# Optimization experiments

Hardware: AMD Instinct MI355X
Metric: run time of the kernel (lower is better)

The kernel has to match this reference:

```python
import jax, jax.numpy as jnp
import numpy as np

FEATS = 1024
HEAD = 16
MLP_HIDDEN = 4096
HEAD_DIM = FEATS // HEAD
SQRT_D = float(FEATS) ** 0.5  # module scales by sqrt(feats), not sqrt(head_dim)
LN_EPS = 1e-5


def layer_norm(x, g, b):
    mu = jnp.mean(x, axis=-1, keepdims=True)
    var = jnp.mean(jnp.square(x - mu), axis=-1, keepdims=True)
    return (x - mu) * jax.lax.rsqrt(var + LN_EPS) * g + b


def setup_inputs() -> dict:
    key = jax.random.key(0)
    ks = jax.random.split(key, 12)
    s = 1.0 / np.sqrt(FEATS)
    s2 = 1.0 / np.sqrt(MLP_HIDDEN)
    return {
        "x": jax.random.normal(ks[0], (2, 2048, FEATS), dtype=jnp.float32),
        "ln1_g": jnp.ones((FEATS,), jnp.float32),
        "ln1_b": jnp.zeros((FEATS,), jnp.float32),
        "wq": jax.random.normal(ks[1], (FEATS, FEATS), jnp.float32) * s,
        "bq": jnp.zeros((FEATS,), jnp.float32),
        "wk": jax.random.normal(ks[2], (FEATS, FEATS), jnp.float32) * s,
        "bk": jnp.zeros((FEATS,), jnp.float32),
        "wv": jax.random.normal(ks[3], (FEATS, FEATS), jnp.float32) * s,
        "bv": jnp.zeros((FEATS,), jnp.float32),
        "wo": jax.random.normal(ks[4], (FEATS, FEATS), jnp.float32) * s,
        "bo": jnp.zeros((FEATS,), jnp.float32),
        "ln2_g": jnp.ones((FEATS,), jnp.float32),
        "ln2_b": jnp.zeros((FEATS,), jnp.float32),
        "w1": jax.random.normal(ks[5], (MLP_HIDDEN, FEATS), jnp.float32) * s,
        "b1": jnp.zeros((MLP_HIDDEN,), jnp.float32),
        "w2": jax.random.normal(ks[6], (FEATS, MLP_HIDDEN), jnp.float32) * s2,
        "b2": jnp.zeros((FEATS,), jnp.float32),
    }


def reference(x, ln1_g, ln1_b, wq, bq, wk, bk, wv, bv, wo, bo,
              ln2_g, ln2_b, w1, b1, w2, b2):
    b, n, f = x.shape
    h = layer_norm(x, ln1_g, ln1_b)
    # qkv projections (torch Linear: y = x @ W.T + b)
    q = (h @ wq.T + bq).reshape(b, n, HEAD, HEAD_DIM).transpose(0, 2, 1, 3)
    k = (h @ wk.T + bk).reshape(b, n, HEAD, HEAD_DIM).transpose(0, 2, 1, 3)
    v = (h @ wv.T + bv).reshape(b, n, HEAD, HEAD_DIM).transpose(0, 2, 1, 3)
    score = jax.nn.softmax(jnp.einsum('bhif,bhjf->bhij', q, k) / SQRT_D, axis=-1)
    attn = jnp.einsum('bhij,bhjf->bihf', score, v).reshape(b, n, f)
    o = attn @ wo.T + bo
    out1 = o + x
    h2 = layer_norm(out1, ln2_g, ln2_b)
    mlp = jax.nn.relu(jax.nn.relu(h2 @ w1.T + b1) @ w2.T + b2)
    return mlp + out1
```

## Files before the change

kernel.cpp:

```cpp
#include <hip/hip_runtime.h>
#include <hip/hip_bf16.h>

#define FEATS 1024
#define NH 16
#define HD 64
#define SEQ 2048
#define BATCH 2
#define MTOT (BATCH*SEQ)
#define MLPH 4096

typedef __attribute__((ext_vector_type(8))) short bf16x8;
typedef __attribute__((ext_vector_type(4))) float f32x4;

static_assert(sizeof(bf16x8) == 16, "bf16x8 must be 16B");

__device__ __forceinline__ unsigned short f2bf(float f) {
    unsigned int u = __float_as_uint(f);
    unsigned int lsb = (u >> 16) & 1u;
    u += 0x7fffu + lsb;
    return (unsigned short)(u >> 16);
}

#define ASYNC16(GP, LP) __builtin_amdgcn_global_load_lds( \
    (const __attribute__((address_space(1))) void*)(GP),  \
    (__attribute__((address_space(3))) void*)(LP), 16, 0, 0)

__global__ __launch_bounds__(256) void cvt_kernel(const float* __restrict__ src,
                                                  unsigned short* __restrict__ dst, int n) {
    int i = (blockIdx.x * 256 + threadIdx.x) * 4;
    if (i + 3 < n) {
        float4 v = *(const float4*)(src + i);
        ushort4 o;
        o.x = f2bf(v.x); o.y = f2bf(v.y); o.z = f2bf(v.z); o.w = f2bf(v.w);
        *(ushort4*)(dst + i) = o;
    }
}

__global__ __launch_bounds__(256) void concat3_kernel(const float* __restrict__ a,
                                                      const float* __restrict__ b,
                                                      const float* __restrict__ c,
                                                      float* __restrict__ o) {
    int i = blockIdx.x * 256 + threadIdx.x;
    float v = (i < 1024) ? a[i] : ((i < 2048) ? b[i - 1024] : c[i - 2048]);
    o[i] = v;
}

__global__ __launch_bounds__(256) void ln_kernel(const float* __restrict__ x,
                                                 const float* __restrict__ g,
                                                 const float* __restrict__ bta,
                                                 unsigned short* __restrict__ h) {
    __shared__ float red[8];
    const int row = blockIdx.x;
    const int t = threadIdx.x;
    const float* xr = x + (size_t)row * FEATS;
    float4 v = ((const float4*)xr)[t];
    float s  = v.x + v.y + v.z + v.w;
    float ss = v.x * v.x + v.y * v.y + v.z * v.z + v.w * v.w;
#pragma unroll
    for (int off = 1; off < 64; off <<= 1) {
        s  += __shfl_xor(s, off);
        ss += __shfl_xor(ss, off);
    }
    const int w = t >> 6;
    if ((t & 63) == 0) { red[w] = s; red[4 + w] = ss; }
    __syncthreads();
    s  = red[0] + red[1] + red[2] + red[3];
    ss = red[4] + red[5] + red[6] + red[7];
    const float mu  = s * (1.f / FEATS);
    const float var = ss * (1.f / FEATS) - mu * mu;
    const float rs  = rsqrtf(var + 1e-5f);
    float4 gv = ((const float4*)g)[t];
    float4 bv = ((const float4*)bta)[t];
    ushort4 ov;
    ov.x = f2bf((v.x - mu) * rs * gv.x + bv.x);
    ov.y = f2bf((v.y - mu) * rs * gv.y + bv.y);
    ov.z = f2bf((v.z - mu) * rs * gv.z + bv.z);
    ov.w = f2bf((v.w - mu) * rs * gv.w + bv.w);
    ((ushort4*)h)[(size_t)row * (FEATS / 4) + t] = ov;
}

template <bool RELU, bool ADD, bool OUTBF16>
__global__ __launch_bounds__(256, 2)
void gemm_kernel(const unsigned short* __restrict__ A,
                 const unsigned short* __restrict__ W,
                 const float* __restrict__ bias,
                 const float* __restrict__ addend,
                 void* __restrict__ outp,
                 int M, int N, int K, int gx) {
    __shared__ unsigned short lds[3][2][128 * 32];

    const int t = threadIdx.x;
    const int w = t >> 6, lane = t & 63;
    const int wr = w >> 1, wc = w & 1;
    const int li = lane & 15, lj = lane >> 4;

    const int nwg = gridDim.x;
    const int cpx = nwg >> 3;
    const int wg = blockIdx.x;
    const int swz = (wg & 7) * cpx + (wg >> 3);
    const int mb = (swz / gx) * 128, nb = (swz % gx) * 128;

    const int srow = lane >> 2, sc = (lane & 3) * 8;
    const unsigned short* gA = A + (size_t)(mb + w * 16 + srow) * K + sc;
    const unsigned short* gB = W + (size_t)(nb + w * 16 + srow) * K + sc;
    const size_t half = (size_t)64 * K;
    const int lbase = w * 512 + lane * 8;

    const int nt = K >> 5;

#define STAGE(BUF, K0)                                             \
    do {                                                           \
        unsigned short* la_ = &lds[BUF][0][lbase];                 \
        unsigned short* lb_ = &lds[BUF][1][lbase];                 \
        ASYNC16(gA + (K0), la_);                                   \
        ASYNC16(gA + half + (K0), la_ + 2048);                     \
        ASYNC16(gB + (K0), lb_);                                   \
        ASYNC16(gB + half + (K0), lb_ + 2048);                     \
    } while (0)

    STAGE(0, 0);
    STAGE(1, 32);
    asm volatile("s_waitcnt vmcnt(4)" ::: "memory");
    __builtin_amdgcn_s_barrier();

    f32x4 acc[4][4] = {};

    for (int i = 0; i < nt; ++i) {
        const int cur = i % 3;
        const unsigned short* Al = &lds[cur][0][0];
        const unsigned short* Bl = &lds[cur][1][0];

        bf16x8 af[4], bfr[4];
#pragma unroll
        for (int m = 0; m < 4; m++)
            af[m] = *(const bf16x8*)(Al + (wr * 64 + m * 16 + li) * 32 + lj * 8);
#pragma unroll
        for (int n = 0; n < 4; n++)
            bfr[n] = *(const bf16x8*)(Bl + (wc * 64 + n * 16 + li) * 32 + lj * 8);

        const int pf = i + 2 < nt;
        if (pf) STAGE((i + 2) % 3, (i + 2) * 32);

#pragma unroll
        for (int m = 0; m < 4; m++)
#pragma unroll
            for (int n = 0; n < 4; n++)
                acc[m][n] = __builtin_amdgcn_mfma_f32_16x16x32_bf16(af[m], bfr[n], acc[m][n], 0, 0, 0);

        if (i + 1 < nt) {
            if (pf) asm volatile("s_waitcnt vmcnt(4)" ::: "memory");
            else    asm volatile("s_waitcnt vmcnt(0)" ::: "memory");
            __builtin_amdgcn_s_barrier();
        }
    }
#undef STAGE

#pragma unroll
    for (int m = 0; m < 4; m++) {
#pragma unroll
        for (int n = 0; n < 4; n++) {
            const int col = nb + wc * 64 + n * 16 + li;
            const float bv = bias[col];
#pragma unroll
            for (int r = 0; r < 4; r++) {
                const int row = mb + wr * 64 + m * 16 + lj * 4 + r;
                float v = acc[m][n][r] + bv;
                if (RELU) v = fmaxf(v, 0.f);
                if (ADD)  v += addend[(size_t)row * N + col];
                if (OUTBF16)
                    ((unsigned short*)outp)[(size_t)row * N + col] = f2bf(v);
                else
                    ((float*)outp)[(size_t)row * N + col] = v;
            }
        }
    }
}

__global__ __launch_bounds__(256) void vtrans_kernel(const unsigned short* __restrict__ qkv,
                                                     unsigned short* __restrict__ vt) {
    constexpr int LDV = 68;
    __shared__ unsigned short Vl[64 * LDV];
    const int bh = blockIdx.x, st = blockIdx.y;
    const int b = bh >> 4, h = bh & 15;
    const int t = threadIdx.x;
    const unsigned short* src = qkv + (size_t)(b * SEQ + st * 64) * (3 * FEATS) + 2 * FEATS + h * HD;
#pragma unroll
    for (int i = 0; i < 2; i++) {
        int idx = t + i * 256;
        int r = idx >> 3, c = (idx & 7) * 8;
        *(bf16x8*)(Vl + r * LDV + c) = *(const bf16x8*)(src + (size_t)r * (3 * FEATS) + c);
    }
    __syncthreads();
    unsigned short* dst = vt + (size_t)bh * HD * SEQ + st * 64;
#pragma unroll
    for (int i = 0; i < 2; i++) {
        int idx = t + i * 256;
        int d = idx >> 3, s8 = (idx & 7) * 8;
        bf16x8 v;
#pragma unroll
        for (int j = 0; j < 8; j++) v[j] = Vl[(s8 + j) * LDV + d];
        *(bf16x8*)(dst + (size_t)d * SEQ + s8) = v;
    }
}

__global__ __launch_bounds__(512, 2)
void attn_kernel(const unsigned short* __restrict__ qkv,
                 const unsigned short* __restrict__ vt,
                 unsigned short* __restrict__ out) {
    constexpr int LK = 72;
    constexpr int LP = 68;
    __shared__ unsigned short Kl[64 * LK];
    __shared__ unsigned short Vtl[64 * LK];
    __shared__ unsigned short Pl[8][16 * LP];

    const int bh = blockIdx.x;
    const int b = bh >> 4, h = bh & 15;
    const int q0 = blockIdx.y * 128;
    const int t = threadIdx.x, w = t >> 6, lane = t & 63;
    const int li = lane & 15, lj = lane >> 4;

    const size_t rstr = 3 * FEATS;
    const unsigned short* qkvb = qkv + (size_t)(b * SEQ) * rstr;
    const unsigned short* ksrc = qkvb + FEATS + h * HD;
    const unsigned short* vsrc = vt + (size_t)bh * HD * SEQ;

    bf16x8 aq[2];
#pragma unroll
    for (int kk = 0; kk < 2; kk++)
        aq[kk] = *(const bf16x8*)(qkvb + (size_t)(q0 + w * 16 + li) * rstr + h * HD + kk * 32 + lj * 8);

    f32x4 o[4] = {};
    float lsum[4] = {0.f, 0.f, 0.f, 0.f};
    const float c2 = 1.4426950408889634f / 32.0f;

    const int sr = t >> 3, scol = (t & 7) * 8;

    for (int kv0 = 0; kv0 < SEQ; kv0 += 64) {
        __syncthreads();
        *(bf16x8*)(Kl + sr * LK + scol) =
            *(const bf16x8*)(ksrc + (size_t)(kv0 + sr) * rstr + scol);
        *(bf16x8*)(Vtl + sr * LK + scol) =
            *(const bf16x8*)(vsrc + (size_t)sr * SEQ + kv0 + scol);
        __syncthreads();

        f32x4 s[4];
#pragma unroll
        for (int n = 0; n < 4; n++) {
            bf16x8 b0 = *(const bf16x8*)(Kl + (n * 16 + li) * LK + lj * 8);
            bf16x8 b1 = *(const bf16x8*)(Kl + (n * 16 + li) * LK + 32 + lj * 8);
            f32x4 acc = {};
            acc = __builtin_amdgcn_mfma_f32_16x16x32_bf16(aq[0], b0, acc, 0, 0, 0);
            acc = __builtin_amdgcn_mfma_f32_16x16x32_bf16(aq[1], b1, acc, 0, 0, 0);
            s[n] = acc;
        }

#pragma unroll
        for (int n = 0; n < 4; n++)
#pragma unroll
            for (int r = 0; r < 4; r++) {
                float p = exp2f(s[n][r] * c2);
                lsum[r] += p;
                Pl[w][(lj * 4 + r) * LP + n * 16 + li] = f2bf(p);
            }

#pragma unroll
        for (int kk = 0; kk < 2; kk++) {
            bf16x8 ap = *(const bf16x8*)(Pl[w] + li * LP + kk * 32 + lj * 8);
#pragma unroll
            for (int n = 0; n < 4; n++) {
                bf16x8 bv = *(const bf16x8*)(Vtl + (n * 16 + li) * LK + kk * 32 + lj * 8);
                o[n] = __builtin_amdgcn_mfma_f32_16x16x32_bf16(ap, bv, o[n], 0, 0, 0);
            }
        }
    }

    float inv[4];
#pragma unroll
    for (int r = 0; r < 4; r++) {
        float s = lsum[r];
        s += __shfl_xor(s, 1);
        s += __shfl_xor(s, 2);
        s += __shfl_xor(s, 4);
        s += __shfl_xor(s, 8);
        inv[r] = 1.f / s;
    }
    unsigned short* ob = out + (size_t)(b * SEQ + q0 + w * 16) * FEATS + h * HD;
#pragma unroll
    for (int n = 0; n < 4; n++)
#pragma unroll
        for (int r = 0; r < 4; r++)
            ob[(size_t)(lj * 4 + r) * FEATS + n * 16 + li] = f2bf(o[n][r] * inv[r]);
}

extern "C" void kernel_launch(void* const* d_in, const int* in_sizes, int n_in,
                              void* d_out, int out_size, void* d_ws, size_t ws_size,
                              hipStream_t stream) {
    const float* x     = (const float*)d_in[0];
    const float* ln1_g = (const float*)d_in[1];
    const float* ln1_b = (const float*)d_in[2];
    const float* wq    = (const float*)d_in[3];
    const float* bq    = (const float*)d_in[4];
    const float* wk    = (const float*)d_in[5];
    const float* bk    = (const float*)d_in[6];
    const float* wv    = (const float*)d_in[7];
    const float* bvv   = (const float*)d_in[8];
    const float* wo    = (const float*)d_in[9];
    const float* bo    = (const float*)d_in[10];
    const float* ln2_g = (const float*)d_in[11];
    const float* ln2_b = (const float*)d_in[12];
    const float* w1    = (const float*)d_in[13];
    const float* b1    = (const float*)d_in[14];
    const float* w2    = (const float*)d_in[15];
    const float* b2    = (const float*)d_in[16];

    unsigned short* wqkv_b = (unsigned short*)d_ws;
    unsigned short* wo_b   = wqkv_b + 3072 * 1024;
    unsigned short* w1_b   = wo_b + 1024 * 1024;
    unsigned short* w2_b   = w1_b + 4096 * 1024;
    float*          bqkv   = (float*)(w2_b + 1024 * 4096);
    unsigned short* region = (unsigned short*)(bqkv + 3072);
    unsigned short* qkvb   = region;
    unsigned short* hb     = region + (size_t)4096 * 3072;
    unsigned short* vtb    = hb;
    unsigned short* a1     = region;
    unsigned short* attn_o = region + (size_t)4096 * 4096;
    unsigned short* h2     = attn_o;
    float*          out1   = (float*)(attn_o + (size_t)4096 * 1024);
    float*          outf   = (float*)d_out;

    dim3 blk(256);

    cvt_kernel<<<1024, blk, 0, stream>>>(wq, wqkv_b, 1024 * 1024);
    cvt_kernel<<<1024, blk, 0, stream>>>(wk, wqkv_b + 1024 * 1024, 1024 * 1024);
    cvt_kernel<<<1024, blk, 0, stream>>>(wv, wqkv_b + 2 * 1024 * 1024, 1024 * 1024);
    cvt_kernel<<<1024, blk, 0, stream>>>(wo, wo_b, 1024 * 1024);
    cvt_kernel<<<4096, blk, 0, stream>>>(w1, w1_b, 4096 * 1024);
    cvt_kernel<<<4096, blk, 0, stream>>>(w2, w2_b, 4096 * 1024);
    concat3_kernel<<<12, blk, 0, stream>>>(bq, bk, bvv, bqkv);

    ln_kernel<<<MTOT, blk, 0, stream>>>(x, ln1_g, ln1_b, hb);

    gemm_kernel<false, false, true><<<768, blk, 0, stream>>>(
        hb, wqkv_b, bqkv, nullptr, qkvb, MTOT, 3072, FEATS, 24);

    vtrans_kernel<<<dim3(BATCH * NH, SEQ / 64), blk, 0, stream>>>(qkvb, vtb);

    attn_kernel<<<dim3(BATCH * NH, SEQ / 128), dim3(512), 0, stream>>>(qkvb, vtb, attn_o);

    gemm_kernel<false, true, false><<<256, blk, 0, stream>>>(
        attn_o, wo_b, bo, x, out1, MTOT, FEATS, FEATS, 8);

    ln_kernel<<<MTOT, blk, 0, stream>>>(out1, ln2_g, ln2_b, h2);

    gemm_kernel<true, false, true><<<1024, blk, 0, stream>>>(
        h2, w1_b, b1, nullptr, a1, MTOT, MLPH, FEATS, 32);

    gemm_kernel<true, true, false><<<256, blk, 0, stream>>>(
        a1, w2_b, b2, out1, outf, MTOT, FEATS, MLPH, 8);
}
```

Baseline: 262.9 us.

## Triple-buffer attention K/V tiles with async LDS loads and transposed P reads

Reworks the attention inner loop to stage K and V^T tiles into a three-deep LDS ring using async global-to-LDS loads, prefetching two tiles ahead. This replaces the synchronous load-then-barrier pattern, aiming to hide global latency. It also adds XOR-swizzled LDS layouts in place of padding, packed bf16 conversion of P, ds_read_b64_tr_b16 transposed reads for the P operand, and priority hints around the MFMA sections. Launch bounds are raised to 4 blocks per CU, which constrains registers and relies on the LDS footprint fitting, with added complexity in the waitcnt accounting.

Result: no change. 266.3 us (+1.3%).

```diff
diff --git a/kernel.cpp b/kernel.cpp
--- a/kernel.cpp
+++ b/kernel.cpp
@@ -10,6 +10,7 @@
 #define MLPH 4096
 
 typedef __attribute__((ext_vector_type(8))) short bf16x8;
+typedef __attribute__((ext_vector_type(4))) short bf16x4;
 typedef __attribute__((ext_vector_type(4))) float f32x4;
 
 static_assert(sizeof(bf16x8) == 16, "bf16x8 must be 16B");
@@ -203,26 +204,35 @@
     }
 }
 
-__global__ __launch_bounds__(512, 2)
+__global__ __launch_bounds__(512, 4)
 void attn_kernel(const unsigned short* __restrict__ qkv,
                  const unsigned short* __restrict__ vt,
                  unsigned short* __restrict__ out) {
-    constexpr int LK = 72;
-    constexpr int LP = 68;
-    __shared__ unsigned short Kl[64 * LK];
-    __shared__ unsigned short Vtl[64 * LK];
-    __shared__ unsigned short Pl[8][16 * LP];
+    __shared__ unsigned short Kl[3][64 * 64];
+    __shared__ unsigned short Vtl[3][64 * 64];
+    __shared__ unsigned short Pt[8][64 * 16];
 
     const int bh = blockIdx.x;
     const int b = bh >> 4, h = bh & 15;
     const int q0 = blockIdx.y * 128;
     const int t = threadIdx.x, w = t >> 6, lane = t & 63;
     const int li = lane & 15, lj = lane >> 4;
+    const int e7 = li & 7;
 
     const size_t rstr = 3 * FEATS;
     const unsigned short* qkvb = qkv + (size_t)(b * SEQ) * rstr;
-    const unsigned short* ksrc = qkvb + FEATS + h * HD;
-    const unsigned short* vsrc = vt + (size_t)bh * HD * SEQ;
+
+    const int sr = t >> 3;
+    const int sslot = (t & 7) ^ (sr & 7);
+    const unsigned short* kBase = qkvb + FEATS + h * HD + (size_t)sr * rstr + sslot * 8;
+    const unsigned short* vBase = vt + (size_t)bh * HD * SEQ + (size_t)sr * SEQ + sslot * 8;
+    const int ldst = t * 8;
+
+#define STAGEA(BUF, KV0)                                    \
+    do {                                                    \
+        ASYNC16(kBase + (size_t)(KV0) * rstr, &Kl[BUF][ldst]); \
+        ASYNC16(vBase + (KV0), &Vtl[BUF][ldst]);            \
+    } while (0)
 
     bf16x8 aq[2];
 #pragma unroll
@@ -233,56 +243,105 @@
     float lsum[4] = {0.f, 0.f, 0.f, 0.f};
     const float c2 = 1.4426950408889634f / 32.0f;
 
-    const int sr = t >> 3, scol = (t & 7) * 8;
-
-    for (int kv0 = 0; kv0 < SEQ; kv0 += 64) {
-        __syncthreads();
-        *(bf16x8*)(Kl + sr * LK + scol) =
-            *(const bf16x8*)(ksrc + (size_t)(kv0 + sr) * rstr + scol);
-        *(bf16x8*)(Vtl + sr * LK + scol) =
-            *(const bf16x8*)(vsrc + (size_t)sr * SEQ + kv0 + scol);
-        __syncthreads();
+    unsigned short* Ptw = &Pt[w][0];
+    const unsigned ptoff =
+        (unsigned)(size_t)(__attribute__((address_space(3))) void*)Ptw;
+    const unsigned paddr = ptoff + (unsigned)(li * 2 + lj * 128);
+
+    const int nt = SEQ / 64;
+    STAGEA(0, 0);
+    STAGEA(1, 64);
+    asm volatile("s_waitcnt vmcnt(2)" ::: "memory");
+    __builtin_amdgcn_s_barrier();
+
+    for (int i = 0; i < nt; ++i) {
+        const unsigned short* Kc = Kl[i % 3];
+        const unsigned short* Vc = Vtl[i % 3];
+
+        const int pf = i + 2 < nt;
+        if (pf) STAGEA((i + 2) % 3, (i + 2) * 64);
 
         f32x4 s[4];
+        __builtin_amdgcn_s_setprio(1);
 #pragma unroll
         for (int n = 0; n < 4; n++) {
-            bf16x8 b0 = *(const bf16x8*)(Kl + (n * 16 + li) * LK + lj * 8);
-            bf16x8 b1 = *(const bf16x8*)(Kl + (n * 16 + li) * LK + 32 + lj * 8);
+            const int row = n * 16 + li;
+            bf16x8 b0 = *(const bf16x8*)(Kc + row * 64 + ((lj ^ e7) * 8));
+            bf16x8 b1 = *(const bf16x8*)(Kc + row * 64 + (((lj + 4) ^ e7) * 8));
             f32x4 acc = {};
             acc = __builtin_amdgcn_mfma_f32_16x16x32_bf16(aq[0], b0, acc, 0, 0, 0);
             acc = __builtin_amdgcn_mfma_f32_16x16x32_bf16(aq[1], b1, acc, 0, 0, 0);
             s[n] = acc;
         }
-
-#pragma unroll
-        for (int n = 0; n < 4; n++)
-#pragma unroll
-            for (int r = 0; r < 4; r++) {
-                float p = exp2f(s[n][r] * c2);
-                lsum[r] += p;
-                Pl[w][(lj * 4 + r) * LP + n * 16 + li] = f2bf(p);
+        __builtin_amdgcn_s_setprio(0);
+
+#pragma unroll
+        for (int n = 0; n < 4; n++) {
+            float p0 = exp2f(s[n][0] * c2);
+            float p1 = exp2f(s[n][1] * c2);
+            float p2 = exp2f(s[n][2] * c2);
+            float p3 = exp2f(s[n][3] * c2);
+            lsum[0] += p0; lsum[1] += p1; lsum[2] += p2; lsum[3] += p3;
+            unsigned w0, w1;
+            asm("v_cvt_pk_bf16_f32 %0, %1, %2" : "=v"(w0) : "v"(p0), "v"(p1));
+            asm("v_cvt_pk_bf16_f32 %0, %1, %2" : "=v"(w1) : "v"(p2), "v"(p3));
+            uint2 pk; pk.x = w0; pk.y = w1;
+            *(uint2*)(Ptw + (n * 16 + li) * 16 + lj * 4) = pk;
+        }
+
+        asm volatile("s_waitcnt lgkmcnt(0)" ::: "memory");
+        __builtin_amdgcn_sched_barrier(0);
+        bf16x4 pa0, pa1, pa2, pa3;
+        asm volatile("ds_read_b64_tr_b16 %0, %4 offset:0\n\t"
+                     "ds_read_b64_tr_b16 %1, %4 offset:512\n\t"
+                     "ds_read_b64_tr_b16 %2, %4 offset:1024\n\t"
+                     "ds_read_b64_tr_b16 %3, %4 offset:1536"
+                     : "=&v"(pa0), "=&v"(pa1), "=&v"(pa2), "=&v"(pa3)
+                     : "v"(paddr));
+        bf16x8 A0 = __builtin_shufflevector(pa0, pa1, 0, 1, 2, 3, 4, 5, 6, 7);
+        bf16x8 A1 = __builtin_shufflevector(pa2, pa3, 0, 1, 2, 3, 4, 5, 6, 7);
+
+        bf16x8 bv[4][2];
+#pragma unroll
+        for (int n = 0; n < 4; n++) {
+            const int row = n * 16 + li;
+#pragma unroll
+            for (int kk = 0; kk < 2; kk++) {
+                bf16x4 vlo = *(const bf16x4*)(Vc + row * 64 +
+                    (((kk * 4 + (lj >> 1)) ^ e7) * 8) + (lj & 1) * 4);
+                bf16x4 vhi = *(const bf16x4*)(Vc + row * 64 +
+                    (((kk * 4 + 2 + (lj >> 1)) ^ e7) * 8) + (lj & 1) * 4);
+                bv[n][kk] = __builtin_shufflevector(vlo, vhi, 0, 1, 2, 3, 4, 5, 6, 7);
             }
-
-#pragma unroll
-        for (int kk = 0; kk < 2; kk++) {
-            bf16x8 ap = *(const bf16x8*)(Pl[w] + li * LP + kk * 32 + lj * 8);
-#pragma unroll
-            for (int n = 0; n < 4; n++) {
-                bf16x8 bv = *(const bf16x8*)(Vtl + (n * 16 + li) * LK + kk * 32 + lj * 8);
-                o[n] = __builtin_amdgcn_mfma_f32_16x16x32_bf16(ap, bv, o[n], 0, 0, 0);
-            }
-        }
-    }
+        }
+        asm volatile("s_waitcnt lgkmcnt(0)" ::: "memory");
+        __builtin_amdgcn_sched_barrier(0);
+
+        __builtin_amdgcn_s_setprio(1);
+#pragma unroll
+        for (int n = 0; n < 4; n++) {
+            o[n] = __builtin_amdgcn_mfma_f32_16x16x32_bf16(A0, bv[n][0], o[n], 0, 0, 0);
+            o[n] = __builtin_amdgcn_mfma_f32_16x16x32_bf16(A1, bv[n][1], o[n], 0, 0, 0);
+        }
+        __builtin_amdgcn_s_setprio(0);
+
+        if (i + 1 < nt) {
+            if (pf) asm volatile("s_waitcnt vmcnt(2)" ::: "memory");
+            else    asm volatile("s_waitcnt vmcnt(0)" ::: "memory");
+            __builtin_amdgcn_s_barrier();
+        }
+    }
+#undef STAGEA
 
     float inv[4];
 #pragma unroll
     for (int r = 0; r < 4; r++) {
-        float s = lsum[r];
-        s += __shfl_xor(s, 1);
-        s += __shfl_xor(s, 2);
-        s += __shfl_xor(s, 4);
-        s += __shfl_xor(s, 8);
-        inv[r] = 1.f / s;
+        float sred = lsum[r];
+        sred += __shfl_xor(sred, 1);
+        sred += __shfl_xor(sred, 2);
+        sred += __shfl_xor(sred, 4);
+        sred += __shfl_xor(sred, 8);
+        inv[r] = 1.f / sred;
     }
     unsigned short* ob = out + (size_t)(b * SEQ + q0 + w * 16) * FEATS + h * HD;
 #pragma unroll
```

## Double-buffer K/V tiles in attention with register prefetch and raise occupancy bounds

Applied to the files above, without the earlier changes.

The attention kernel now keeps two LDS buffers for K and V^T and loads the next tile into registers while the current tile is computed, then stores it to the other buffer. This cuts the per-iteration pair of barriers to one and hides global load latency behind the MFMA work. It also raises launch_bounds minimum occupancy for the GEMM (2 to 3 blocks) and attention (2 to 4 blocks) kernels, and adds s_setprio around the MFMA sections. The higher occupancy targets limit registers per thread and could cause spills. The doubled LDS use could also stop the attention kernel from reaching the requested occupancy.

Result: no change. 259.9 us (-1.1%).

```diff
diff --git a/kernel.cpp b/kernel.cpp
--- a/kernel.cpp
+++ b/kernel.cpp
@@ -80,7 +80,7 @@
 }
 
 template <bool RELU, bool ADD, bool OUTBF16>
-__global__ __launch_bounds__(256, 2)
+__global__ __launch_bounds__(256, 3)
 void gemm_kernel(const unsigned short* __restrict__ A,
                  const unsigned short* __restrict__ W,
                  const float* __restrict__ bias,
@@ -203,14 +203,14 @@
     }
 }
 
-__global__ __launch_bounds__(512, 2)
+__global__ __launch_bounds__(512, 4)
 void attn_kernel(const unsigned short* __restrict__ qkv,
                  const unsigned short* __restrict__ vt,
                  unsigned short* __restrict__ out) {
     constexpr int LK = 72;
     constexpr int LP = 68;
-    __shared__ unsigned short Kl[64 * LK];
-    __shared__ unsigned short Vtl[64 * LK];
+    __shared__ unsigned short Kl[2][64 * LK];
+    __shared__ unsigned short Vtl[2][64 * LK];
     __shared__ unsigned short Pl[8][16 * LP];
 
     const int bh = blockIdx.x;
@@ -234,25 +234,45 @@
     const float c2 = 1.4426950408889634f / 32.0f;
 
     const int sr = t >> 3, scol = (t & 7) * 8;
-
-    for (int kv0 = 0; kv0 < SEQ; kv0 += 64) {
-        __syncthreads();
-        *(bf16x8*)(Kl + sr * LK + scol) =
-            *(const bf16x8*)(ksrc + (size_t)(kv0 + sr) * rstr + scol);
-        *(bf16x8*)(Vtl + sr * LK + scol) =
-            *(const bf16x8*)(vsrc + (size_t)sr * SEQ + kv0 + scol);
-        __syncthreads();
+    const unsigned short* kg = ksrc + (size_t)sr * rstr + scol;
+    const unsigned short* vg = vsrc + (size_t)sr * SEQ + scol;
+    const int ldo = sr * LK + scol;
+
+    const int nt = SEQ / 64;
+
+    {
+        bf16x8 k0 = *(const bf16x8*)kg;
+        bf16x8 v0 = *(const bf16x8*)vg;
+        *(bf16x8*)(&Kl[0][ldo])  = k0;
+        *(bf16x8*)(&Vtl[0][ldo]) = v0;
+    }
+
+    int cur = 0;
+    for (int i = 0; i < nt; ++i) {
+        bf16x8 kreg, vreg;
+        if (i + 1 < nt) {
+            kreg = *(const bf16x8*)(kg + (size_t)(i + 1) * 64 * rstr);
+            vreg = *(const bf16x8*)(vg + (i + 1) * 64);
+        }
+
+        asm volatile("s_waitcnt lgkmcnt(0)" ::: "memory");
+        __builtin_amdgcn_s_barrier();
+
+        const unsigned short* Kc = Kl[cur];
+        const unsigned short* Vc = Vtl[cur];
 
         f32x4 s[4];
+        __builtin_amdgcn_s_setprio(1);
 #pragma unroll
         for (int n = 0; n < 4; n++) {
-            bf16x8 b0 = *(const bf16x8*)(Kl + (n * 16 + li) * LK + lj * 8);
-            bf16x8 b1 = *(const bf16x8*)(Kl + (n * 16 + li) * LK + 32 + lj * 8);
+            bf16x8 b0 = *(const bf16x8*)(Kc + (n * 16 + li) * LK + lj * 8);
+            bf16x8 b1 = *(const bf16x8*)(Kc + (n * 16 + li) * LK + 32 + lj * 8);
             f32x4 acc = {};
             acc = __builtin_amdgcn_mfma_f32_16x16x32_bf16(aq[0], b0, acc, 0, 0, 0);
             acc = __builtin_amdgcn_mfma_f32_16x16x32_bf16(aq[1], b1, acc, 0, 0, 0);
             s[n] = acc;
         }
+        __builtin_amdgcn_s_setprio(0);
 
 #pragma unroll
         for (int n = 0; n < 4; n++)
@@ -263,26 +283,34 @@
                 Pl[w][(lj * 4 + r) * LP + n * 16 + li] = f2bf(p);
             }
 
+        __builtin_amdgcn_s_setprio(1);
 #pragma unroll
         for (int kk = 0; kk < 2; kk++) {
             bf16x8 ap = *(const bf16x8*)(Pl[w] + li * LP + kk * 32 + lj * 8);
 #pragma unroll
             for (int n = 0; n < 4; n++) {
-                bf16x8 bv = *(const bf16x8*)(Vtl + (n * 16 + li) * LK + kk * 32 + lj * 8);
+                bf16x8 bv = *(const bf16x8*)(Vc + (n * 16 + li) * LK + kk * 32 + lj * 8);
                 o[n] = __builtin_amdgcn_mfma_f32_16x16x32_bf16(ap, bv, o[n], 0, 0, 0);
             }
         }
+        __builtin_amdgcn_s_setprio(0);
+
+        if (i + 1 < nt) {
+            *(bf16x8*)(&Kl[cur ^ 1][ldo])  = kreg;
+            *(bf16x8*)(&Vtl[cur ^ 1][ldo]) = vreg;
+        }
+        cur ^= 1;
     }
 
     float inv[4];
 #pragma unroll
     for (int r = 0; r < 4; r++) {
-        float s = lsum[r];
-        s += __shfl_xor(s, 1);
-        s += __shfl_xor(s, 2);
-        s += __shfl_xor(s, 4);
-        s += __shfl_xor(s, 8);
-        inv[r] = 1.f / s;
+        float sred = lsum[r];
+        sred += __shfl_xor(sred, 1);
+        sred += __shfl_xor(sred, 2);
+        sred += __shfl_xor(sred, 4);
+        sred += __shfl_xor(sred, 8);
+        inv[r] = 1.f / sred;
     }
     unsigned short* ob = out + (size_t)(b * SEQ + q0 + w * 16) * FEATS + h * HD;
 #pragma unroll
```
